# Kernel optimization log

Measured on AMD Instinct MI355X. Metric: run time of the kernel, lower is better.

The kernel has to match this reference:

```python
import jax, jax.numpy as jnp
import numpy as np

N, E = 50000, 800000
C_IN, C_HID, C_OUT = 64, 128, 64
BN_EPS = 1e-5


def setup_inputs() -> dict:
    key = jax.random.key(0)
    ks = jax.random.split(key, 8)
    s1 = 1.0 / np.sqrt(C_IN)
    s2 = 1.0 / np.sqrt(C_HID)
    return {
        "x": jax.random.normal(ks[0], (N, C_IN), dtype=jnp.float32),
        "edge_index": jax.random.randint(ks[1], (2, E), 0, N, dtype=jnp.int64),
        # message MLP: in -> hidden -> out
        "W1": jax.random.uniform(ks[2], (C_IN, C_HID), jnp.float32, -s1, s1),
        "b1": jnp.zeros((C_HID,), jnp.float32),
        "W2": jax.random.uniform(ks[3], (C_HID, C_OUT), jnp.float32, -s2, s2),
        "b2": jnp.zeros((C_OUT,), jnp.float32),
        # root/self transform
        "W_root": jax.random.uniform(ks[4], (C_IN, C_OUT), jnp.float32, -s1, s1),
        "b_root": jnp.zeros((C_OUT,), jnp.float32),
        # PReLU (single shared parameter, torch default 0.25)
        "prelu_w": jnp.full((1,), 0.25, jnp.float32),
        # BatchNorm affine params
        "bn_gamma": jnp.ones((C_OUT,), jnp.float32),
        "bn_beta": jnp.zeros((C_OUT,), jnp.float32),
    }


def reference(x, edge_index, W1, b1, W2, b2, W_root, b_root, prelu_w, bn_gamma, bn_beta):
    src, dst = edge_index[0], edge_index[1]
    # gather -> per-edge message MLP: [E, C_hid] -> [E, C_out]
    m = jax.nn.relu(x[src] @ W1 + b1) @ W2 + b2
    # scatter-sum to destination nodes: [N, C_out]
    agg = jax.ops.segment_sum(m, dst, num_segments=N)
    h = agg + x @ W_root + b_root
    # PReLU
    h = jnp.where(h >= 0, h, prelu_w * h)
    # BatchNorm over nodes (training-mode batch stats, biased var)
    mu = jnp.mean(h, axis=0)
    var = jnp.mean(jnp.square(h - mu), axis=0)
    h = (h - mu) * jax.lax.rsqrt(var + BN_EPS) * bn_gamma + bn_beta
    return h
```

## Files before the change

kernel.cpp:

```cpp
#include <hip/hip_runtime.h>

#define NNODES 50000
#define NEDGES 800000
#define NTILES 3125
#define CAP    64

typedef __attribute__((ext_vector_type(8))) short bf16x8;
typedef __attribute__((ext_vector_type(4))) float f32x4;

union FragU { uint u[4]; bf16x8 v; };

__device__ __forceinline__ uint bfr(float f) {
    uint u = __float_as_uint(f);
    return (u + 0x7fffu + ((u >> 16) & 1u)) >> 16;
}
__device__ __forceinline__ uint pack_bf2(float a, float b) {
    return bfr(a) | (bfr(b) << 16);
}
__device__ __forceinline__ float bf2f(uint hi16) {
    return __uint_as_float(hi16 << 16);
}

__global__ __launch_bounds__(256) void prep_kernel(
    const float* __restrict__ W1, const float* __restrict__ b1,
    const float* __restrict__ W2, const float* __restrict__ b2,
    const float* __restrict__ Wr, const float* __restrict__ br,
    uint* __restrict__ tbl)
{
    const int f = blockIdx.x;
    const int tid = threadIdx.x;
    if (f < 40) {
        const int ln = tid >> 2, dd = tid & 3;
        const int g = ln >> 4, r = ln & 15;
        const int j0 = 2 * dd;
        float w0, w1v;
        if (f < 16) {
            const int mt = f >> 1, ks = f & 1;
            const int k = 32 * ks + 8 * g + j0, c = 16 * mt + r;
            w0 = W1[k * 128 + c];  w1v = W1[(k + 1) * 128 + c];
        } else if (f < 32) {
            const int mt = (f - 16) >> 2, ks = (f - 16) & 3;
            const int k = 32 * ks + 8 * g + j0, c = 16 * mt + r;
            w0 = W2[k * 64 + c];   w1v = W2[(k + 1) * 64 + c];
        } else {
            const int mt = (f - 32) >> 1, ks = (f - 32) & 1;
            const int k = 32 * ks + 8 * g + j0, c = 16 * mt + r;
            w0 = Wr[k * 64 + c];   w1v = Wr[(k + 1) * 64 + c];
        }
        tbl[f * 256 + tid] = pack_bf2(w0, w1v);
    } else {
        if (tid < 128) tbl[10240 + tid] = __float_as_uint(b1[tid]);
        if (tid < 64) {
            tbl[10368 + tid] = __float_as_uint(b2[tid]);
            tbl[10432 + tid] = __float_as_uint(br[tid]);
        }
    }
}

__global__ __launch_bounds__(256) void mlp_root_kernel(
    const float* __restrict__ x, const uint* __restrict__ tbl,
    ushort* __restrict__ M16, float* __restrict__ R)
{
    __shared__ uint sTab[10496];
    __shared__ uint sH[4 * 16 * 68];

    const int tid = threadIdx.x;
    {
        uint4* s4 = (uint4*)sTab;
        const uint4* t4 = (const uint4*)tbl;
        for (int i = tid; i < 2624; i += 256) s4[i] = t4[i];
    }
    __syncthreads();
    const uint*  sFrag = sTab;
    const float* sb1 = (const float*)&sTab[10240];
    const float* sb2 = (const float*)&sTab[10368];
    const float* sbr = (const float*)&sTab[10432];

    const int lane = tid & 63;
    const int g = lane >> 4, r = lane & 15;
    uint* Hw = &sH[(tid >> 6) * 16 * 68];
    uint* Mu = (uint*)M16;
    const int gw  = blockIdx.x * 4 + (tid >> 6);
    const int nwv = gridDim.x * 4;

#define LOADFRAG(f) (*(const bf16x8*)&sFrag[((f) << 8) | (lane << 2)])

    for (int t = gw; t < NTILES; t += nwv) {
        const int node = t * 16 + r;
        bf16x8 xf[2];
#pragma unroll
        for (int ks = 0; ks < 2; ++ks) {
            const float4 f0 = *(const float4*)&x[node * 64 + 32 * ks + 8 * g];
            const float4 f1 = *(const float4*)&x[node * 64 + 32 * ks + 8 * g + 4];
            FragU fx;
            fx.u[0] = pack_bf2(f0.x, f0.y); fx.u[1] = pack_bf2(f0.z, f0.w);
            fx.u[2] = pack_bf2(f1.x, f1.y); fx.u[3] = pack_bf2(f1.z, f1.w);
            xf[ks] = fx.v;
        }
#pragma unroll
        for (int mt = 0; mt < 8; ++mt) {
            f32x4 a = {0.f, 0.f, 0.f, 0.f};
            a = __builtin_amdgcn_mfma_f32_16x16x32_bf16(LOADFRAG(2 * mt), xf[0], a, 0, 0, 0);
            a = __builtin_amdgcn_mfma_f32_16x16x32_bf16(LOADFRAG(2 * mt + 1), xf[1], a, 0, 0, 0);
            const int hc = 16 * mt + 4 * g;
            const float v0 = fmaxf(a[0] + sb1[hc + 0], 0.f);
            const float v1 = fmaxf(a[1] + sb1[hc + 1], 0.f);
            const float v2 = fmaxf(a[2] + sb1[hc + 2], 0.f);
            const float v3 = fmaxf(a[3] + sb1[hc + 3], 0.f);
            const int hd = r * 68 + 8 * mt + 2 * g;
            Hw[hd]     = pack_bf2(v0, v1);
            Hw[hd + 1] = pack_bf2(v2, v3);
        }
        bf16x8 hf[4];
#pragma unroll
        for (int ks = 0; ks < 4; ++ks)
            hf[ks] = *(const bf16x8*)&Hw[r * 68 + 16 * ks + 4 * g];
#pragma unroll
        for (int mt = 0; mt < 4; ++mt) {
            f32x4 a2 = {0.f, 0.f, 0.f, 0.f};
#pragma unroll
            for (int ks = 0; ks < 4; ++ks)
                a2 = __builtin_amdgcn_mfma_f32_16x16x32_bf16(LOADFRAG(16 + 4 * mt + ks), hf[ks], a2, 0, 0, 0);
            f32x4 ar = {0.f, 0.f, 0.f, 0.f};
            ar = __builtin_amdgcn_mfma_f32_16x16x32_bf16(LOADFRAG(32 + 2 * mt), xf[0], ar, 0, 0, 0);
            ar = __builtin_amdgcn_mfma_f32_16x16x32_bf16(LOADFRAG(32 + 2 * mt + 1), xf[1], ar, 0, 0, 0);
            const int oc = 16 * mt + 4 * g;
            const float m0 = a2[0] + sb2[oc + 0], m1 = a2[1] + sb2[oc + 1];
            const float m2 = a2[2] + sb2[oc + 2], m3 = a2[3] + sb2[oc + 3];
            uint2 mp = make_uint2(pack_bf2(m0, m1), pack_bf2(m2, m3));
            *(uint2*)&Mu[node * 32 + 8 * mt + 2 * g] = mp;
            float4 rv = make_float4(ar[0] + sbr[oc + 0], ar[1] + sbr[oc + 1],
                                    ar[2] + sbr[oc + 2], ar[3] + sbr[oc + 3]);
            *(float4*)&R[node * 64 + oc] = rv;
        }
    }
#undef LOADFRAG
}

__global__ __launch_bounds__(256) void fill_kernel(
    const int* __restrict__ ei, int* __restrict__ cnt, ushort* __restrict__ bucketU)
{
    const int e = blockIdx.x * 256 + threadIdx.x;
    const int dst = ei[NEDGES + e];
    const int pos = atomicAdd(&cnt[dst], 1);
    if (pos < CAP) bucketU[dst * CAP + pos] = (ushort)ei[e];
}

__global__ __launch_bounds__(256) void gather_prelu_stats_kernel(
    const int* __restrict__ cnt, const ushort* __restrict__ bucketU,
    const uint* __restrict__ M32, const float* __restrict__ pw,
    float* __restrict__ h, float* __restrict__ stats)
{
    __shared__ float ls[128];
    const int tid = threadIdx.x;
    if (tid < 128) ls[tid] = 0.f;
    __syncthreads();

    const int lane = tid & 63;
    const int half = lane >> 5;
    const int dw   = lane & 31;
    const int gw   = (blockIdx.x * 256 + tid) >> 6;
    const int nwv  = (gridDim.x * 256) >> 6;
    const float p  = pw[0];
    float sum = 0.f, sumsq = 0.f;

    for (int n = gw; n < NNODES; n += nwv) {
        int c = cnt[n]; c = c > CAP ? CAP : c;
        const int   sv = (int)bucketU[n * CAP + lane];
        const float hv = h[n * 64 + lane];
        float aL0 = 0.f, aL1 = 0.f, aH0 = 0.f, aH1 = 0.f;
        int i = 0;
        for (; i + 16 <= c; i += 16) {
#pragma unroll
            for (int j = 0; j < 8; ++j) {
                const int s = __shfl(sv, i + 2 * j + half);
                const uint mv = M32[s * 32 + dw];
                if (j & 1) { aL1 += bf2f(mv & 0xffffu); aH1 += bf2f(mv >> 16); }
                else       { aL0 += bf2f(mv & 0xffffu); aH0 += bf2f(mv >> 16); }
            }
        }
        if (i < c) {
#pragma unroll
            for (int j = 0; j < 8; ++j) {
                const int idx = i + 2 * j + half;
                const int s = __shfl(sv, idx & 63);
                if (idx < c) {
                    const uint mv = M32[s * 32 + dw];
                    if (j & 1) { aL1 += bf2f(mv & 0xffffu); aH1 += bf2f(mv >> 16); }
                    else       { aL0 += bf2f(mv & 0xffffu); aH0 += bf2f(mv >> 16); }
                }
            }
        }
        float aL = aL0 + aL1, aH = aH0 + aH1;
        aL += __shfl_xor(aL, 32);
        aH += __shfl_xor(aH, 32);
        const float vlo = __shfl(aL, lane >> 1);
        const float vhi = __shfl(aH, lane >> 1);
        float v = hv + ((lane & 1) ? vhi : vlo);
        v = (v >= 0.f) ? v : p * v;
        h[n * 64 + lane] = v;
        sum += v;
        sumsq = fmaf(v, v, sumsq);
    }
    atomicAdd(&ls[lane], sum);
    atomicAdd(&ls[64 + lane], sumsq);
    __syncthreads();
    if (tid < 128) atomicAdd(&stats[tid], ls[tid]);
}

__global__ __launch_bounds__(256) void bn_kernel(
    float4* __restrict__ h, const float* __restrict__ stats,
    const float* __restrict__ gamma, const float* __restrict__ beta)
{
    const int i  = blockIdx.x * 256 + threadIdx.x;
    const int c0 = (i & 15) * 4;
    const float inv = 1.0f / (float)NNODES;
    const float4 s1 = *(const float4*)&stats[c0];
    const float4 s2 = *(const float4*)&stats[64 + c0];
    const float4 gm = *(const float4*)&gamma[c0];
    const float4 bt = *(const float4*)&beta[c0];
    float4 v = h[i];
    float mu, var;
    mu = s1.x * inv; var = s2.x * inv - mu * mu; v.x = (v.x - mu) * (gm.x * rsqrtf(var + 1e-5f)) + bt.x;
    mu = s1.y * inv; var = s2.y * inv - mu * mu; v.y = (v.y - mu) * (gm.y * rsqrtf(var + 1e-5f)) + bt.y;
    mu = s1.z * inv; var = s2.z * inv - mu * mu; v.z = (v.z - mu) * (gm.z * rsqrtf(var + 1e-5f)) + bt.z;
    mu = s1.w * inv; var = s2.w * inv - mu * mu; v.w = (v.w - mu) * (gm.w * rsqrtf(var + 1e-5f)) + bt.w;
    h[i] = v;
}

extern "C" void kernel_launch(void* const* d_in, const int* in_sizes, int n_in,
                              void* d_out, int out_size, void* d_ws, size_t ws_size,
                              hipStream_t stream) {
    const float* x     = (const float*)d_in[0];
    const int*   ei    = (const int*)d_in[1];
    const float* W1    = (const float*)d_in[2];
    const float* b1    = (const float*)d_in[3];
    const float* W2    = (const float*)d_in[4];
    const float* b2    = (const float*)d_in[5];
    const float* Wr    = (const float*)d_in[6];
    const float* br    = (const float*)d_in[7];
    const float* pw    = (const float*)d_in[8];
    const float* gamma = (const float*)d_in[9];
    const float* beta  = (const float*)d_in[10];

    float* out = (float*)d_out;

    char* ws = (char*)d_ws;
    ushort* M16    = (ushort*)ws;
    ushort* bucketU= (ushort*)(ws + 6400000);
    int*    cnt    = (int*)(ws + 12800000);
    float*  stats  = (float*)(ws + 12800000 + 200000);
    uint*   tbl    = (uint*)(ws + 12800000 + 200000 + 512);

    hipMemsetAsync(cnt, 0, 200000 + 512, stream);

    prep_kernel<<<41, 256, 0, stream>>>(W1, b1, W2, b2, Wr, br, tbl);
    fill_kernel<<<NEDGES / 256, 256, 0, stream>>>(ei, cnt, bucketU);
    mlp_root_kernel<<<512, 256, 0, stream>>>(x, tbl, M16, out);
    gather_prelu_stats_kernel<<<2048, 256, 0, stream>>>(cnt, bucketU, (const uint*)M16, pw, out, stats);
    bn_kernel<<<3125, 256, 0, stream>>>((float4*)out, stats, gamma, beta);
}
```

Baseline: 215.5 us.

## Widen gather loads, prefetch next node, fold memset into prep kernel

The gather kernel now reads each message row with 8-byte uint2 loads, so 16 lanes cover a row and four edges are handled per wave step. The first 32 edges are loaded unconditionally into registers before accumulation to raise memory-level parallelism. The next node's count, bucket and root row are prefetched while the current node is processed. The separate memset is replaced by extra prep_kernel blocks that zero cnt and stats, saving one launch. The cost is more shuffle reductions, higher register pressure, and wasted loads for low-degree nodes.

New measurement: 214.1 us. No clear change (-0.7%).

```diff
diff --git a/kernel.cpp b/kernel.cpp
--- a/kernel.cpp
+++ b/kernel.cpp
@@ -25,7 +25,7 @@
     const float* __restrict__ W1, const float* __restrict__ b1,
     const float* __restrict__ W2, const float* __restrict__ b2,
     const float* __restrict__ Wr, const float* __restrict__ br,
-    uint* __restrict__ tbl)
+    uint* __restrict__ tbl, int* __restrict__ cnt, float* __restrict__ stats)
 {
     const int f = blockIdx.x;
     const int tid = threadIdx.x;
@@ -48,12 +48,16 @@
             w0 = Wr[k * 64 + c];   w1v = Wr[(k + 1) * 64 + c];
         }
         tbl[f * 256 + tid] = pack_bf2(w0, w1v);
-    } else {
+    } else if (f == 40) {
         if (tid < 128) tbl[10240 + tid] = __float_as_uint(b1[tid]);
         if (tid < 64) {
             tbl[10368 + tid] = __float_as_uint(b2[tid]);
             tbl[10432 + tid] = __float_as_uint(br[tid]);
         }
+    } else {
+        const int idx = (f - 41) * 256 + tid;
+        if (idx < NNODES) cnt[idx] = 0;
+        if (f == 41 && tid < 128) stats[tid] = 0.f;
     }
 }
 
@@ -148,7 +152,7 @@
 
 __global__ __launch_bounds__(256) void gather_prelu_stats_kernel(
     const int* __restrict__ cnt, const ushort* __restrict__ bucketU,
-    const uint* __restrict__ M32, const float* __restrict__ pw,
+    const uint2* __restrict__ M8, const float* __restrict__ pw,
     float* __restrict__ h, float* __restrict__ stats)
 {
     __shared__ float ls[128];
@@ -157,46 +161,81 @@
     __syncthreads();
 
     const int lane = tid & 63;
-    const int half = lane >> 5;
-    const int dw   = lane & 31;
+    const int q    = lane >> 4;
+    const int u    = lane & 15;
     const int gw   = (blockIdx.x * 256 + tid) >> 6;
     const int nwv  = (gridDim.x * 256) >> 6;
     const float p  = pw[0];
     float sum = 0.f, sumsq = 0.f;
 
+    int   cN  = 0, svN = 0;
+    float hvN = 0.f;
+    if (gw < NNODES) {
+        cN  = cnt[gw];
+        svN = (int)bucketU[gw * 64 + lane];
+        hvN = h[gw * 64 + lane];
+    }
+
     for (int n = gw; n < NNODES; n += nwv) {
-        int c = cnt[n]; c = c > CAP ? CAP : c;
-        const int   sv = (int)bucketU[n * CAP + lane];
-        const float hv = h[n * 64 + lane];
-        float aL0 = 0.f, aL1 = 0.f, aH0 = 0.f, aH1 = 0.f;
-        int i = 0;
-        for (; i + 16 <= c; i += 16) {
-#pragma unroll
-            for (int j = 0; j < 8; ++j) {
-                const int s = __shfl(sv, i + 2 * j + half);
-                const uint mv = M32[s * 32 + dw];
-                if (j & 1) { aL1 += bf2f(mv & 0xffffu); aH1 += bf2f(mv >> 16); }
-                else       { aL0 += bf2f(mv & 0xffffu); aH0 += bf2f(mv >> 16); }
+        int c = cN; c = c > CAP ? CAP : c;
+        const int   sv = svN;
+        const float hv = hvN;
+
+        uint2 mv[8];
+#pragma unroll
+        for (int j = 0; j < 8; ++j) {
+            const int idx = 4 * j + q;
+            const int s = __shfl(sv, (idx < c) ? idx : 0);
+            mv[j] = M8[s * 16 + u];
+        }
+
+        const int nn = n + nwv;
+        if (nn < NNODES) {
+            cN  = cnt[nn];
+            svN = (int)bucketU[nn * 64 + lane];
+            hvN = h[nn * 64 + lane];
+        }
+
+        float a0 = 0.f, a1 = 0.f, a2 = 0.f, a3 = 0.f;
+        float b0 = 0.f, b1 = 0.f, b2 = 0.f, b3 = 0.f;
+#pragma unroll
+        for (int j = 0; j < 8; ++j) {
+            const bool ok = (4 * j + q) < c;
+            const uint lo = ok ? mv[j].x : 0u;
+            const uint hi = ok ? mv[j].y : 0u;
+            if (j & 1) {
+                b0 += bf2f(lo & 0xffffu); b1 += bf2f(lo >> 16);
+                b2 += bf2f(hi & 0xffffu); b3 += bf2f(hi >> 16);
+            } else {
+                a0 += bf2f(lo & 0xffffu); a1 += bf2f(lo >> 16);
+                a2 += bf2f(hi & 0xffffu); a3 += bf2f(hi >> 16);
             }
         }
-        if (i < c) {
-#pragma unroll
-            for (int j = 0; j < 8; ++j) {
-                const int idx = i + 2 * j + half;
-                const int s = __shfl(sv, idx & 63);
-                if (idx < c) {
-                    const uint mv = M32[s * 32 + dw];
-                    if (j & 1) { aL1 += bf2f(mv & 0xffffu); aH1 += bf2f(mv >> 16); }
-                    else       { aL0 += bf2f(mv & 0xffffu); aH0 += bf2f(mv >> 16); }
-                }
+        if (c > 32) {
+            for (int i = 32; i < c; i += 4) {
+                const int idx = i + q;
+                const int s = __shfl(sv, (idx < c) ? idx : 0);
+                const uint2 m = M8[s * 16 + u];
+                const bool ok = idx < c;
+                const uint lo = ok ? m.x : 0u;
+                const uint hi = ok ? m.y : 0u;
+                a0 += bf2f(lo & 0xffffu); a1 += bf2f(lo >> 16);
+                a2 += bf2f(hi & 0xffffu); a3 += bf2f(hi >> 16);
             }
         }
-        float aL = aL0 + aL1, aH = aH0 + aH1;
-        aL += __shfl_xor(aL, 32);
-        aH += __shfl_xor(aH, 32);
-        const float vlo = __shfl(aL, lane >> 1);
-        const float vhi = __shfl(aH, lane >> 1);
-        float v = hv + ((lane & 1) ? vhi : vlo);
+        a0 += b0; a1 += b1; a2 += b2; a3 += b3;
+
+        a0 += __shfl_xor(a0, 16); a0 += __shfl_xor(a0, 32);
+        a1 += __shfl_xor(a1, 16); a1 += __shfl_xor(a1, 32);
+        a2 += __shfl_xor(a2, 16); a2 += __shfl_xor(a2, 32);
+        a3 += __shfl_xor(a3, 16); a3 += __shfl_xor(a3, 32);
+
+        const int srcl = lane >> 2;
+        const float t0 = __shfl(a0, srcl), t1 = __shfl(a1, srcl);
+        const float t2 = __shfl(a2, srcl), t3 = __shfl(a3, srcl);
+        const float e01 = (lane & 1) ? t1 : t0;
+        const float e23 = (lane & 1) ? t3 : t2;
+        float v = hv + ((lane & 2) ? e23 : e01);
         v = (v >= 0.f) ? v : p * v;
         h[n * 64 + lane] = v;
         sum += v;
@@ -252,11 +291,9 @@
     float*  stats  = (float*)(ws + 12800000 + 200000);
     uint*   tbl    = (uint*)(ws + 12800000 + 200000 + 512);
 
-    hipMemsetAsync(cnt, 0, 200000 + 512, stream);
-
-    prep_kernel<<<41, 256, 0, stream>>>(W1, b1, W2, b2, Wr, br, tbl);
+    prep_kernel<<<237, 256, 0, stream>>>(W1, b1, W2, b2, Wr, br, tbl, cnt, stats);
     fill_kernel<<<NEDGES / 256, 256, 0, stream>>>(ei, cnt, bucketU);
     mlp_root_kernel<<<512, 256, 0, stream>>>(x, tbl, M16, out);
-    gather_prelu_stats_kernel<<<2048, 256, 0, stream>>>(cnt, bucketU, (const uint*)M16, pw, out, stats);
+    gather_prelu_stats_kernel<<<2048, 256, 0, stream>>>(cnt, bucketU, (const uint2*)M16, pw, out, stats);
     bn_kernel<<<3125, 256, 0, stream>>>((float4*)out, stats, gamma, beta);
 }
```
